# Kernel optimization log

Measured on AMD Instinct MI355X. Metric: run time of the kernel, lower is better.

Reference implementation:

```python
import jax, jax.numpy as jnp
import numpy as np

H = 16  # hidden_size
D = 32  # input_size == output_size
B = 2048
T = 512


def _leaky(x):
    return jnp.where(x >= 0, x, 0.01 * x)  # nn.LeakyReLU default slope


def _lstm_cell(x, h, c, Wih, Whh, bih, bhh):
    # torch.nn.LSTMCell gate order: i, f, g, o
    g = x @ Wih.T + h @ Whh.T + bih + bhh  # [B, 4H]
    i, f, gg, o = jnp.split(g, 4, axis=-1)
    i = jax.nn.sigmoid(i)
    f = jax.nn.sigmoid(f)
    gg = jnp.tanh(gg)
    o = jax.nn.sigmoid(o)
    c = f * c + i * gg
    h = o * jnp.tanh(c)
    return h, c


def setup_inputs() -> dict:
    key = jax.random.key(0)
    ks = jax.random.split(key, 20)
    s = 1.0 / np.sqrt(H)
    u = lambda k, shape: jax.random.uniform(k, shape, jnp.float32, -s, s)
    return {
        "seq": jax.random.normal(ks[0], (B, T, D), jnp.float32),
        "pre_w1": u(ks[1], (H, D)), "pre_b1": u(ks[2], (H,)),
        "pre_w2": u(ks[3], (H, H)), "pre_b2": u(ks[4], (H,)),
        "pre_w3": u(ks[5], (H, H)), "pre_b3": u(ks[6], (H,)),
        "enc_Wih": u(ks[7], (4 * H, H)), "enc_Whh": u(ks[8], (4 * H, H)),
        "enc_bih": u(ks[9], (4 * H,)), "enc_bhh": u(ks[10], (4 * H,)),
        "h2l_w1": u(ks[11], (H, H)), "h2l_b1": u(ks[12], (H,)),
        "h2l_w2": u(ks[13], (H, H)), "h2l_b2": u(ks[14], (H,)),
        "post_w": u(ks[15], (D, H)), "post_b": u(ks[16], (D,)),
    }


def reference(seq, pre_w1, pre_b1, pre_w2, pre_b2, pre_w3, pre_b3,
              enc_Wih, enc_Whh, enc_bih, enc_bhh,
              h2l_w1, h2l_b1, h2l_w2, h2l_b2, post_w, post_b):
    Bx = seq.shape[0]
    # pre MLP: Linear -> LeakyReLU -> Linear -> LeakyReLU -> Linear
    x = _leaky(seq @ pre_w1.T + pre_b1)
    x = _leaky(x @ pre_w2.T + pre_b2)
    x = x @ pre_w3.T + pre_b3  # [B, T, H]

    start0 = x[:, -1, :]
    h0 = jnp.zeros((Bx, H), seq.dtype)
    c0 = jnp.zeros((Bx, H), seq.dtype)

    # encoder loop over time (serial)
    def enc_step(carry, xt):
        h, c = carry
        h, c = _lstm_cell(xt, h, c, enc_Wih, enc_Whh, enc_bih, enc_bhh)
        return (h, c), None

    (h, c), _ = jax.lax.scan(enc_step, (h0, c0), jnp.swapaxes(x, 0, 1))

    # decoder loop (note: source reuses self.encoder cell here)
    def dec_step(carry, _):
        h, c, start = carry
        h, c = _lstm_cell(start, h, c, enc_Wih, enc_Whh, enc_bih, enc_bhh)
        start = _leaky(h @ h2l_w1.T + h2l_b1) @ h2l_w2.T + h2l_b2
        out = h @ post_w.T + post_b  # [B, D]
        return (h, c, start), out

    _, outs = jax.lax.scan(dec_step, (h, c, start0), None, length=seq.shape[1])
    # outputs[:, -1 - i] = out_i  ->  reverse time, then [B, T, D]
    outputs = jnp.swapaxes(outs[::-1], 0, 1)
    return (outputs, outputs)
```

## Files before the change

kernel.cpp:

```cpp
#include <hip/hip_runtime.h>

#define T_LEN 512
#define OSTRIDE ((size_t)2048 * 512 * 32)

typedef float v2f __attribute__((ext_vector_type(2)));
#define PKFMA(a, b, c) __builtin_elementwise_fma((a), (b), (c))

__device__ __forceinline__ float rlf(float v, int l) {
  return __int_as_float(__builtin_amdgcn_readlane(__float_as_int(v), l));
}
#define QB(v, pat) __int_as_float(__builtin_amdgcn_mov_dpp(__float_as_int(v), (pat), 0xF, 0xF, false))

__global__ __launch_bounds__(64) void setup_kernel(
    const float* __restrict__ Wih, const float* __restrict__ bih,
    const float* __restrict__ bhh, const float* __restrict__ w3,
    const float* __restrict__ b3, float* __restrict__ Wz,
    float* __restrict__ Bz) {
  const int g = threadIdx.x;
  const float sK = ((g >> 4) == 2) ? 2.0f : -1.0f;
  float acc[16];
#pragma unroll
  for (int k = 0; k < 16; ++k) acc[k] = 0.f;
  float bz = bih[g] + bhh[g];
#pragma unroll
  for (int j = 0; j < 16; ++j) {
    const float wij = Wih[g * 16 + j];
#pragma unroll
    for (int k = 0; k < 16; ++k)
      acc[k] = __builtin_fmaf(wij, w3[j * 16 + k], acc[k]);
    bz = __builtin_fmaf(wij, b3[j], bz);
  }
#pragma unroll
  for (int k = 0; k < 16; ++k) Wz[g * 16 + k] = sK * acc[k];
  Bz[g] = sK * bz;
}

__global__ __launch_bounds__(256) void prenet_y2_kernel(
    const float* __restrict__ seq,
    const float* __restrict__ w1, const float* __restrict__ b1,
    const float* __restrict__ w2, const float* __restrict__ b2,
    const float* __restrict__ w3, const float* __restrict__ b3,
    float* __restrict__ y2g, float* __restrict__ xstart) {
  const int tid = threadIdx.x;
  const size_t r = (size_t)blockIdx.x * 256 + tid;

  const float* sp = seq + r * 32;
  float in[32];
#pragma unroll
  for (int q = 0; q < 8; ++q) {
    float4 v = ((const float4*)sp)[q];
    in[q * 4 + 0] = v.x;
    in[q * 4 + 1] = v.y;
    in[q * 4 + 2] = v.z;
    in[q * 4 + 3] = v.w;
  }

  float y1[16];
#pragma unroll
  for (int j = 0; j < 16; ++j) {
    float a0 = b1[j], a1 = 0.f, a2 = 0.f, a3 = 0.f;
#pragma unroll
    for (int k = 0; k < 32; k += 4) {
      a0 = __builtin_fmaf(w1[j * 32 + k + 0], in[k + 0], a0);
      a1 = __builtin_fmaf(w1[j * 32 + k + 1], in[k + 1], a1);
      a2 = __builtin_fmaf(w1[j * 32 + k + 2], in[k + 2], a2);
      a3 = __builtin_fmaf(w1[j * 32 + k + 3], in[k + 3], a3);
    }
    float s = (a0 + a1) + (a2 + a3);
    y1[j] = s >= 0.f ? s : 0.01f * s;
  }

  float y2[16];
#pragma unroll
  for (int j = 0; j < 16; ++j) {
    float a0 = b2[j], a1 = 0.f, a2 = 0.f, a3 = 0.f;
#pragma unroll
    for (int k = 0; k < 16; k += 4) {
      a0 = __builtin_fmaf(w2[j * 16 + k + 0], y1[k + 0], a0);
      a1 = __builtin_fmaf(w2[j * 16 + k + 1], y1[k + 1], a1);
      a2 = __builtin_fmaf(w2[j * 16 + k + 2], y1[k + 2], a2);
      a3 = __builtin_fmaf(w2[j * 16 + k + 3], y1[k + 3], a3);
    }
    float s = (a0 + a1) + (a2 + a3);
    y2[j] = s >= 0.f ? s : 0.01f * s;
  }

  float* op = y2g + r * 16;
#pragma unroll
  for (int q = 0; q < 4; ++q)
    ((float4*)op)[q] = make_float4(y2[q * 4 + 0], y2[q * 4 + 1],
                                   y2[q * 4 + 2], y2[q * 4 + 3]);

  if ((r & (T_LEN - 1)) == (T_LEN - 1)) {
    float y3[16];
#pragma unroll
    for (int j = 0; j < 16; ++j) {
      float a0 = b3[j], a1 = 0.f, a2 = 0.f, a3 = 0.f;
#pragma unroll
      for (int k = 0; k < 16; k += 4) {
        a0 = __builtin_fmaf(w3[j * 16 + k + 0], y2[k + 0], a0);
        a1 = __builtin_fmaf(w3[j * 16 + k + 1], y2[k + 1], a1);
        a2 = __builtin_fmaf(w3[j * 16 + k + 2], y2[k + 2], a2);
        a3 = __builtin_fmaf(w3[j * 16 + k + 3], y2[k + 3], a3);
      }
      y3[j] = (a0 + a1) + (a2 + a3);
    }
    float* xs = xstart + (r >> 9) * 16;
#pragma unroll
    for (int q = 0; q < 4; ++q)
      ((float4*)xs)[q] = make_float4(y3[q * 4 + 0], y3[q * 4 + 1],
                                     y3[q * 4 + 2], y3[q * 4 + 3]);
  }
}

#define ACTBODY()                                                           \
  do {                                                                      \
    float ee = __expf(g);                                                   \
    float rr = __builtin_amdgcn_rcpf(1.0f + ee);                            \
    float act = __builtin_fmaf(sa, rr, sb);                                 \
    float ii = QB(act, 0x00);                                               \
    float ff = QB(act, 0x55);                                               \
    float gg = QB(act, 0xAA);                                               \
    float oo = QB(act, 0xFF);                                               \
    c = __builtin_fmaf(ff, c, ii * gg);                                     \
    float th = __builtin_fmaf(                                              \
        -2.0f, __builtin_amdgcn_rcpf(1.0f + __expf(c + c)), 1.0f);          \
    h = oo * th;                                                            \
    _Pragma("unroll") for (int m = 0; m < 8; ++m) {                         \
      hk2[m].x = rlf(h, 8 * m);                                             \
      hk2[m].y = rlf(h, 8 * m + 4);                                         \
    }                                                                       \
  } while (0)

#define CELLZ(ZV)                                                           \
  do {                                                                      \
    v2f A, Bv;                                                              \
    A.x = (ZV); A.y = 0.f; Bv.x = 0.f; Bv.y = 0.f;                          \
    _Pragma("unroll") for (int m = 0; m < 8; m += 2) {                      \
      A = PKFMA(whh2[m], hk2[m], A);                                        \
      Bv = PKFMA(whh2[m + 1], hk2[m + 1], Bv);                              \
    }                                                                       \
    float g = (A.x + A.y) + (Bv.x + Bv.y);                                  \
    ACTBODY();                                                              \
  } while (0)

#define CELL(WX2, XA2, BB)                                                  \
  do {                                                                      \
    v2f A, Bv;                                                              \
    A.x = (BB); A.y = 0.f; Bv.x = 0.f; Bv.y = 0.f;                          \
    _Pragma("unroll") for (int m = 0; m < 8; m += 2) {                      \
      A = PKFMA(WX2[m], XA2[m], A);                                         \
      Bv = PKFMA(WX2[m + 1], XA2[m + 1], Bv);                               \
    }                                                                       \
    _Pragma("unroll") for (int m = 0; m < 8; m += 2) {                      \
      A = PKFMA(whh2[m], hk2[m], A);                                        \
      Bv = PKFMA(whh2[m + 1], hk2[m + 1], Bv);                              \
    }                                                                       \
    float g = (A.x + A.y) + (Bv.x + Bv.y);                                  \
    ACTBODY();                                                              \
  } while (0)

#define ZGEMV(YQ, OUTV)                                                     \
  do {                                                                      \
    v2f A, Bv;                                                              \
    A.x = bz; A.y = 0.f; Bv.x = 0.f; Bv.y = 0.f;                            \
    _Pragma("unroll") for (int q = 0; q < 4; ++q) {                         \
      float4 v = (YQ)[q];                                                   \
      v2f ylo, yhi;                                                         \
      ylo.x = v.x; ylo.y = v.y; yhi.x = v.z; yhi.y = v.w;                   \
      A = PKFMA(wz2[2 * q + 0], ylo, A);                                    \
      Bv = PKFMA(wz2[2 * q + 1], yhi, Bv);                                  \
    }                                                                       \
    OUTV = (A.x + A.y) + (Bv.x + Bv.y);                                     \
  } while (0)

__global__ __launch_bounds__(256, 2) void lstm_rec_z_kernel(
    const float* __restrict__ Whh, const float* __restrict__ Wih,
    const float* __restrict__ bih, const float* __restrict__ bhh,
    const float* __restrict__ hw1, const float* __restrict__ hb1,
    const float* __restrict__ hw2, const float* __restrict__ hb2,
    const float* __restrict__ pw, const float* __restrict__ pb,
    const float* __restrict__ Wz, const float* __restrict__ Bz,
    const float* __restrict__ y2g, const float* __restrict__ xstart,
    float* __restrict__ out) {
  const int lane = threadIdx.x & 63;
  const int bu =
      __builtin_amdgcn_readfirstlane(blockIdx.x * 4 + (threadIdx.x >> 6));
  const int hr = lane >> 2;
  const int gi = (lane & 3) * 16 + hr;
  const bool isT = (lane & 3) == 2;

  const float sK = isT ? 2.0f : -1.0f;
  const float sa = isT ? -2.0f : 1.0f;
  const float sb = isT ? 1.0f : 0.0f;

  v2f whh2[8];
#pragma unroll
  for (int m = 0; m < 8; ++m) {
    whh2[m].x = Whh[gi * 16 + 2 * m + 0] * sK;
    whh2[m].y = Whh[gi * 16 + 2 * m + 1] * sK;
  }

  v2f wz2[8];
  {
    const float4* wzv = (const float4*)(Wz + gi * 16);
#pragma unroll
    for (int q = 0; q < 4; ++q) {
      float4 v = wzv[q];
      wz2[2 * q + 0].x = v.x;
      wz2[2 * q + 0].y = v.y;
      wz2[2 * q + 1].x = v.z;
      wz2[2 * q + 1].y = v.w;
    }
  }
  const float bz = Bz[gi];

  float h = 0.f, c = 0.f;
  v2f hk2[8];
#pragma unroll
  for (int m = 0; m < 8; ++m) { hk2[m].x = 0.f; hk2[m].y = 0.f; }

  const float4* yb = (const float4*)(y2g + (size_t)bu * (T_LEN * 16));
  float4 yq[4][4];
#pragma unroll
  for (int u = 0; u < 4; ++u) {
#pragma unroll
    for (int q = 0; q < 4; ++q) yq[u][q] = yb[u * 4 + q];
  }
  __builtin_amdgcn_sched_barrier(0);

  for (int t0 = 0; t0 < T_LEN; t0 += 4) {
#pragma unroll
    for (int u = 0; u < 4; ++u) {
      float zv;
      ZGEMV(yq[u], zv);
      CELLZ(zv);
      int tn = t0 + u + 4;
      tn = tn < T_LEN ? tn : (T_LEN - 1);
#pragma unroll
      for (int q = 0; q < 4; ++q) yq[u][q] = yb[(size_t)tn * 4 + q];
      __builtin_amdgcn_sched_barrier(0);
    }
  }

  v2f wih2[8];
#pragma unroll
  for (int m = 0; m < 8; ++m) {
    wih2[m].x = Wih[gi * 16 + 2 * m + 0] * sK;
    wih2[m].y = Wih[gi * 16 + 2 * m + 1] * sK;
  }
  const float bias = (bih[gi] + bhh[gi]) * sK;

  const int mrow = (lane < 32) ? lane : (lane & 15);
  const float* msrc = (lane < 32) ? (pw + mrow * 16) : (hw1 + mrow * 16);
  const float mbias = (lane < 32) ? pb[mrow] : hb1[mrow];
  const float sl = (lane < 32) ? 1.0f : 0.01f;
  v2f mr2[8];
#pragma unroll
  for (int m = 0; m < 8; ++m) {
    mr2[m].x = msrc[2 * m + 0];
    mr2[m].y = msrc[2 * m + 1];
  }

  float Mr[16];
#pragma unroll
  for (int k = 0; k < 16; ++k) Mr[k] = 0.f;
#pragma unroll
  for (int j = 0; j < 16; ++j) {
    const float wj = (j & 1) ? wih2[j >> 1].y : wih2[j >> 1].x;
#pragma unroll
    for (int k = 0; k < 16; ++k)
      Mr[k] = __builtin_fmaf(wj, hw2[j * 16 + k], Mr[k]);
  }
  float mbias2 = bias;
#pragma unroll
  for (int j = 0; j < 16; ++j) {
    const float wj = (j & 1) ? wih2[j >> 1].y : wih2[j >> 1].x;
    mbias2 = __builtin_fmaf(wj, hb2[j], mbias2);
  }
  v2f Mr2[8];
#pragma unroll
  for (int m = 0; m < 8; ++m) {
    Mr2[m].x = Mr[2 * m + 0];
    Mr2[m].y = Mr[2 * m + 1];
  }

  v2f xk2[8];
  {
    const float* src = xstart + (size_t)bu * 16;
#pragma unroll
    for (int m = 0; m < 8; ++m) {
      xk2[m].x = src[2 * m + 0];
      xk2[m].y = src[2 * m + 1];
    }
  }

  const size_t obase = (size_t)bu * (T_LEN * 32) + (lane & 31);

  CELL(wih2, xk2, bias);

  for (int t = 0; t < T_LEN; ++t) {
    v2f P, Q;
    P.x = mbias; P.y = 0.f; Q.x = 0.f; Q.y = 0.f;
#pragma unroll
    for (int m = 0; m < 8; m += 2) {
      P = PKFMA(mr2[m], hk2[m], P);
      Q = PKFMA(mr2[m + 1], hk2[m + 1], Q);
    }
    float y0 = (P.x + P.y) + (Q.x + Q.y);
    float yv = fmaxf(y0, y0 * sl);

    if (lane < 32) {
      const size_t off = obase + (size_t)(T_LEN - 1 - t) * 32;
      out[off] = yv;
      out[off + OSTRIDE] = yv;
    }

    if (t + 1 < T_LEN) {
      v2f uk2[8];
#pragma unroll
      for (int m = 0; m < 8; ++m) {
        uk2[m].x = rlf(yv, 32 + 2 * m + 0);
        uk2[m].y = rlf(yv, 32 + 2 * m + 1);
      }
      CELL(Mr2, uk2, mbias2);
    }
  }
}

__device__ __forceinline__ void prenet_row(
    const float* __restrict__ sp,
    const float* __restrict__ w1, const float* __restrict__ b1,
    const float* __restrict__ w2, const float* __restrict__ b2,
    const float* __restrict__ w3, const float* __restrict__ b3,
    float y3[16]) {
  float in[32];
#pragma unroll
  for (int q = 0; q < 8; ++q) {
    float4 v = ((const float4*)sp)[q];
    in[q * 4 + 0] = v.x;
    in[q * 4 + 1] = v.y;
    in[q * 4 + 2] = v.z;
    in[q * 4 + 3] = v.w;
  }
  float y1[16];
#pragma unroll
  for (int j = 0; j < 16; ++j) {
    float a0 = b1[j], a1 = 0.f, a2 = 0.f, a3 = 0.f;
#pragma unroll
    for (int k = 0; k < 32; k += 4) {
      a0 = __builtin_fmaf(w1[j * 32 + k + 0], in[k + 0], a0);
      a1 = __builtin_fmaf(w1[j * 32 + k + 1], in[k + 1], a1);
      a2 = __builtin_fmaf(w1[j * 32 + k + 2], in[k + 2], a2);
      a3 = __builtin_fmaf(w1[j * 32 + k + 3], in[k + 3], a3);
    }
    float s = (a0 + a1) + (a2 + a3);
    y1[j] = s >= 0.f ? s : 0.01f * s;
  }
  float y2[16];
#pragma unroll
  for (int j = 0; j < 16; ++j) {
    float a0 = b2[j], a1 = 0.f, a2 = 0.f, a3 = 0.f;
#pragma unroll
    for (int k = 0; k < 16; k += 4) {
      a0 = __builtin_fmaf(w2[j * 16 + k + 0], y1[k + 0], a0);
      a1 = __builtin_fmaf(w2[j * 16 + k + 1], y1[k + 1], a1);
      a2 = __builtin_fmaf(w2[j * 16 + k + 2], y1[k + 2], a2);
      a3 = __builtin_fmaf(w2[j * 16 + k + 3], y1[k + 3], a3);
    }
    float s = (a0 + a1) + (a2 + a3);
    y2[j] = s >= 0.f ? s : 0.01f * s;
  }
#pragma unroll
  for (int j = 0; j < 16; ++j) {
    float a0 = b3[j], a1 = 0.f, a2 = 0.f, a3 = 0.f;
#pragma unroll
    for (int k = 0; k < 16; k += 4) {
      a0 = __builtin_fmaf(w3[j * 16 + k + 0], y2[k + 0], a0);
      a1 = __builtin_fmaf(w3[j * 16 + k + 1], y2[k + 1], a1);
      a2 = __builtin_fmaf(w3[j * 16 + k + 2], y2[k + 2], a2);
      a3 = __builtin_fmaf(w3[j * 16 + k + 3], y2[k + 3], a3);
    }
    y3[j] = (a0 + a1) + (a2 + a3);
  }
}

__global__ __launch_bounds__(256) void prenet_kernel(
    const float* __restrict__ seq,
    const float* __restrict__ w1, const float* __restrict__ b1,
    const float* __restrict__ w2, const float* __restrict__ b2,
    const float* __restrict__ w3, const float* __restrict__ b3,
    float* __restrict__ xws) {
  const size_t r = (size_t)blockIdx.x * 256 + threadIdx.x;
  float y3[16];
  prenet_row(seq + r * 32, w1, b1, w2, b2, w3, b3, y3);
  float* op = xws + r * 16;
#pragma unroll
  for (int q = 0; q < 4; ++q)
    ((float4*)op)[q] =
        make_float4(y3[q * 4 + 0], y3[q * 4 + 1], y3[q * 4 + 2], y3[q * 4 + 3]);
}

__global__ __launch_bounds__(256, 2) void lstm_rec_kernel(
    const float* __restrict__ Wih, const float* __restrict__ Whh,
    const float* __restrict__ bih, const float* __restrict__ bhh,
    const float* __restrict__ hw1, const float* __restrict__ hb1,
    const float* __restrict__ hw2, const float* __restrict__ hb2,
    const float* __restrict__ pw, const float* __restrict__ pb,
    const float* __restrict__ xws, float* __restrict__ out) {
  const int lane = threadIdx.x & 63;
  const int bu =
      __builtin_amdgcn_readfirstlane(blockIdx.x * 4 + (threadIdx.x >> 6));
  const int hr = lane >> 2;
  const int gi = (lane & 3) * 16 + hr;
  const bool isT = (lane & 3) == 2;

  const float sK = isT ? 2.0f : -1.0f;
  const float sa = isT ? -2.0f : 1.0f;
  const float sb = isT ? 1.0f : 0.0f;

  v2f wih2[8], whh2[8];
#pragma unroll
  for (int m = 0; m < 8; ++m) {
    wih2[m].x = Wih[gi * 16 + 2 * m + 0] * sK;
    wih2[m].y = Wih[gi * 16 + 2 * m + 1] * sK;
    whh2[m].x = Whh[gi * 16 + 2 * m + 0] * sK;
    whh2[m].y = Whh[gi * 16 + 2 * m + 1] * sK;
  }
  const float bias = (bih[gi] + bhh[gi]) * sK;

  float h = 0.f, c = 0.f;
  v2f hk2[8];
#pragma unroll
  for (int m = 0; m < 8; ++m) { hk2[m].x = 0.f; hk2[m].y = 0.f; }

  const float* xb = xws + (size_t)bu * (T_LEN * 16);

  v2f xA2[8], xB2[8];
#pragma unroll
  for (int m = 0; m < 8; ++m) {
    xA2[m].x = xb[2 * m + 0];
    xA2[m].y = xb[2 * m + 1];
  }
  for (int t = 0; t < T_LEN; t += 2) {
    const float* n1 = xb + (size_t)(t + 1) * 16;
#pragma unroll
    for (int m = 0; m < 8; ++m) {
      xB2[m].x = n1[2 * m + 0];
      xB2[m].y = n1[2 * m + 1];
    }
    CELL(wih2, xA2, bias);
    const int t2 = (t + 2 < T_LEN) ? (t + 2) : (T_LEN - 1);
    const float* n2 = xb + (size_t)t2 * 16;
#pragma unroll
    for (int m = 0; m < 8; ++m) {
      xA2[m].x = n2[2 * m + 0];
      xA2[m].y = n2[2 * m + 1];
    }
    CELL(wih2, xB2, bias);
  }

  const int mrow = (lane < 32) ? lane : (lane & 15);
  const float* msrc = (lane < 32) ? (pw + mrow * 16) : (hw1 + mrow * 16);
  const float mbias = (lane < 32) ? pb[mrow] : hb1[mrow];
  const float sl = (lane < 32) ? 1.0f : 0.01f;
  v2f mr2[8];
#pragma unroll
  for (int m = 0; m < 8; ++m) {
    mr2[m].x = msrc[2 * m + 0];
    mr2[m].y = msrc[2 * m + 1];
  }

  float Mr[16];
#pragma unroll
  for (int k = 0; k < 16; ++k) Mr[k] = 0.f;
#pragma unroll
  for (int j = 0; j < 16; ++j) {
    const float wj = (j & 1) ? wih2[j >> 1].y : wih2[j >> 1].x;
#pragma unroll
    for (int k = 0; k < 16; ++k)
      Mr[k] = __builtin_fmaf(wj, hw2[j * 16 + k], Mr[k]);
  }
  float mbias2 = bias;
#pragma unroll
  for (int j = 0; j < 16; ++j) {
    const float wj = (j & 1) ? wih2[j >> 1].y : wih2[j >> 1].x;
    mbias2 = __builtin_fmaf(wj, hb2[j], mbias2);
  }
  v2f Mr2[8];
#pragma unroll
  for (int m = 0; m < 8; ++m) {
    Mr2[m].x = Mr[2 * m + 0];
    Mr2[m].y = Mr[2 * m + 1];
  }

  v2f xk2[8];
  {
    const float* src = xb + (size_t)(T_LEN - 1) * 16;
#pragma unroll
    for (int m = 0; m < 8; ++m) {
      xk2[m].x = src[2 * m + 0];
      xk2[m].y = src[2 * m + 1];
    }
  }

  const size_t obase = (size_t)bu * (T_LEN * 32) + (lane & 31);

  CELL(wih2, xk2, bias);

  for (int t = 0; t < T_LEN; ++t) {
    v2f P, Q;
    P.x = mbias; P.y = 0.f; Q.x = 0.f; Q.y = 0.f;
#pragma unroll
    for (int m = 0; m < 8; m += 2) {
      P = PKFMA(mr2[m], hk2[m], P);
      Q = PKFMA(mr2[m + 1], hk2[m + 1], Q);
    }
    float y0 = (P.x + P.y) + (Q.x + Q.y);
    float yv = fmaxf(y0, y0 * sl);

    if (lane < 32) {
      const size_t off = obase + (size_t)(T_LEN - 1 - t) * 32;
      out[off] = yv;
      out[off + OSTRIDE] = yv;
    }

    if (t + 1 < T_LEN) {
      v2f uk2[8];
#pragma unroll
      for (int m = 0; m < 8; ++m) {
        uk2[m].x = rlf(yv, 32 + 2 * m + 0);
        uk2[m].y = rlf(yv, 32 + 2 * m + 1);
      }
      CELL(Mr2, uk2, mbias2);
    }
  }
}

extern "C" void kernel_launch(void* const* d_in, const int* in_sizes, int n_in,
                              void* d_out, int out_size, void* d_ws, size_t ws_size,
                              hipStream_t stream) {
  const float* seq = (const float*)d_in[0];
  const float* pre_w1 = (const float*)d_in[1];
  const float* pre_b1 = (const float*)d_in[2];
  const float* pre_w2 = (const float*)d_in[3];
  const float* pre_b2 = (const float*)d_in[4];
  const float* pre_w3 = (const float*)d_in[5];
  const float* pre_b3 = (const float*)d_in[6];
  const float* enc_Wih = (const float*)d_in[7];
  const float* enc_Whh = (const float*)d_in[8];
  const float* enc_bih = (const float*)d_in[9];
  const float* enc_bhh = (const float*)d_in[10];
  const float* h2l_w1 = (const float*)d_in[11];
  const float* h2l_b1 = (const float*)d_in[12];
  const float* h2l_w2 = (const float*)d_in[13];
  const float* h2l_b2 = (const float*)d_in[14];
  const float* post_w = (const float*)d_in[15];
  const float* post_b = (const float*)d_in[16];

  const size_t y2bytes = (size_t)2048 * 512 * 16 * 4;
  const size_t xsbytes = (size_t)2048 * 16 * 4;
  const size_t wzbytes = 64 * 16 * 4;
  const size_t need = y2bytes + xsbytes + wzbytes + 64 * 4;

  if (ws_size >= need) {
    float* y2g = (float*)d_ws;
    float* xstart = (float*)((char*)d_ws + y2bytes);
    float* Wz = (float*)((char*)d_ws + y2bytes + xsbytes);
    float* Bz = (float*)((char*)d_ws + y2bytes + xsbytes + wzbytes);

    setup_kernel<<<dim3(1), dim3(64), 0, stream>>>(
        enc_Wih, enc_bih, enc_bhh, pre_w3, pre_b3, Wz, Bz);

    prenet_y2_kernel<<<dim3(4096), dim3(256), 0, stream>>>(
        seq, pre_w1, pre_b1, pre_w2, pre_b2, pre_w3, pre_b3, y2g, xstart);

    lstm_rec_z_kernel<<<dim3(512), dim3(256), 0, stream>>>(
        enc_Whh, enc_Wih, enc_bih, enc_bhh, h2l_w1, h2l_b1, h2l_w2, h2l_b2,
        post_w, post_b, Wz, Bz, y2g, xstart, (float*)d_out);
  } else {
    float* xws = (float*)d_ws;

    prenet_kernel<<<dim3(4096), dim3(256), 0, stream>>>(
        seq, pre_w1, pre_b1, pre_w2, pre_b2, pre_w3, pre_b3, xws);

    lstm_rec_kernel<<<dim3(512), dim3(256), 0, stream>>>(
        enc_Wih, enc_Whh, enc_bih, enc_bhh, h2l_w1, h2l_b1, h2l_w2, h2l_b2,
        post_w, post_b, xws, (float*)d_out);
  }
}
```

Before: 720.7 us.

## Interleave two independent batch rows per wavefront in LSTM recurrence kernel

Each wavefront now runs two batch rows' LSTM recurrences side by side, with separate h/c state and register rings, so the two dependent chains can fill each other's latency gaps (ILP) rather than relying on occupancy. The z GEMV for the next timestep is computed one step ahead, so it overlaps with the current cell update. The grid is halved to 256 blocks with launch bounds of 1 block per SM, which raises register use per thread and lowers occupancy in exchange for more independent work per wave.

```diff
diff --git a/kernel.cpp b/kernel.cpp
--- a/kernel.cpp
+++ b/kernel.cpp
@@ -113,68 +113,74 @@
   }
 }
 
-#define ACTBODY()                                                           \
+#define ACT_P(G, H, C, HK)                                                  \
   do {                                                                      \
-    float ee = __expf(g);                                                   \
-    float rr = __builtin_amdgcn_rcpf(1.0f + ee);                            \
-    float act = __builtin_fmaf(sa, rr, sb);                                 \
-    float ii = QB(act, 0x00);                                               \
-    float ff = QB(act, 0x55);                                               \
-    float gg = QB(act, 0xAA);                                               \
-    float oo = QB(act, 0xFF);                                               \
-    c = __builtin_fmaf(ff, c, ii * gg);                                     \
-    float th = __builtin_fmaf(                                              \
-        -2.0f, __builtin_amdgcn_rcpf(1.0f + __expf(c + c)), 1.0f);          \
-    h = oo * th;                                                            \
+    float ee_ = __expf(G);                                                  \
+    float rr_ = __builtin_amdgcn_rcpf(1.0f + ee_);                          \
+    float act_ = __builtin_fmaf(sa, rr_, sb);                               \
+    float ii_ = QB(act_, 0x00);                                             \
+    float ff_ = QB(act_, 0x55);                                             \
+    float gg_ = QB(act_, 0xAA);                                             \
+    float oo_ = QB(act_, 0xFF);                                             \
+    C = __builtin_fmaf(ff_, C, ii_ * gg_);                                  \
+    float th_ = __builtin_fmaf(                                             \
+        -2.0f, __builtin_amdgcn_rcpf(1.0f + __expf(C + C)), 1.0f);          \
+    H = oo_ * th_;                                                          \
     _Pragma("unroll") for (int m = 0; m < 8; ++m) {                         \
-      hk2[m].x = rlf(h, 8 * m);                                             \
-      hk2[m].y = rlf(h, 8 * m + 4);                                         \
+      HK[m].x = rlf(H, 8 * m);                                              \
+      HK[m].y = rlf(H, 8 * m + 4);                                          \
     }                                                                       \
   } while (0)
 
-#define CELLZ(ZV)                                                           \
+#define CELLZ_P(ZV, H, C, HK)                                               \
   do {                                                                      \
-    v2f A, Bv;                                                              \
-    A.x = (ZV); A.y = 0.f; Bv.x = 0.f; Bv.y = 0.f;                          \
+    v2f A_, B_;                                                             \
+    A_.x = (ZV); A_.y = 0.f; B_.x = 0.f; B_.y = 0.f;                        \
     _Pragma("unroll") for (int m = 0; m < 8; m += 2) {                      \
-      A = PKFMA(whh2[m], hk2[m], A);                                        \
-      Bv = PKFMA(whh2[m + 1], hk2[m + 1], Bv);                              \
+      A_ = PKFMA(whh2[m], HK[m], A_);                                       \
+      B_ = PKFMA(whh2[m + 1], HK[m + 1], B_);                               \
     }                                                                       \
-    float g = (A.x + A.y) + (Bv.x + Bv.y);                                  \
-    ACTBODY();                                                              \
+    float g_ = (A_.x + A_.y) + (B_.x + B_.y);                               \
+    ACT_P(g_, H, C, HK);                                                    \
   } while (0)
 
-#define CELL(WX2, XA2, BB)                                                  \
+#define CELL_P(WX2, XA2, BB, H, C, HK)                                      \
   do {                                                                      \
-    v2f A, Bv;                                                              \
-    A.x = (BB); A.y = 0.f; Bv.x = 0.f; Bv.y = 0.f;                          \
+    v2f A_, B_;                                                             \
+    A_.x = (BB); A_.y = 0.f; B_.x = 0.f; B_.y = 0.f;                        \
     _Pragma("unroll") for (int m = 0; m < 8; m += 2) {                      \
-      A = PKFMA(WX2[m], XA2[m], A);                                         \
-      Bv = PKFMA(WX2[m + 1], XA2[m + 1], Bv);                               \
+      A_ = PKFMA(WX2[m], XA2[m], A_);                                       \
+      B_ = PKFMA(WX2[m + 1], XA2[m + 1], B_);                               \
     }                                                                       \
     _Pragma("unroll") for (int m = 0; m < 8; m += 2) {                      \
-      A = PKFMA(whh2[m], hk2[m], A);                                        \
-      Bv = PKFMA(whh2[m + 1], hk2[m + 1], Bv);                              \
+      A_ = PKFMA(whh2[m], HK[m], A_);                                       \
+      B_ = PKFMA(whh2[m + 1], HK[m + 1], B_);                               \
     }                                                                       \
-    float g = (A.x + A.y) + (Bv.x + Bv.y);                                  \
-    ACTBODY();                                                              \
+    float g_ = (A_.x + A_.y) + (B_.x + B_.y);                               \
+    ACT_P(g_, H, C, HK);                                                    \
   } while (0)
 
-#define ZGEMV(YQ, OUTV)                                                     \
+#define ZGEMV_P(YQ, OUTV)                                                   \
   do {                                                                      \
-    v2f A, Bv;                                                              \
-    A.x = bz; A.y = 0.f; Bv.x = 0.f; Bv.y = 0.f;                            \
+    v2f A_, B_;                                                             \
+    A_.x = bz; A_.y = 0.f; B_.x = 0.f; B_.y = 0.f;                          \
     _Pragma("unroll") for (int q = 0; q < 4; ++q) {                         \
-      float4 v = (YQ)[q];                                                   \
-      v2f ylo, yhi;                                                         \
-      ylo.x = v.x; ylo.y = v.y; yhi.x = v.z; yhi.y = v.w;                   \
-      A = PKFMA(wz2[2 * q + 0], ylo, A);                                    \
-      Bv = PKFMA(wz2[2 * q + 1], yhi, Bv);                                  \
+      float4 v_ = (YQ)[q];                                                  \
+      v2f ylo_, yhi_;                                                       \
+      ylo_.x = v_.x; ylo_.y = v_.y; yhi_.x = v_.z; yhi_.y = v_.w;           \
+      A_ = PKFMA(wz2[2 * q + 0], ylo_, A_);                                 \
+      B_ = PKFMA(wz2[2 * q + 1], yhi_, B_);                                 \
     }                                                                       \
-    OUTV = (A.x + A.y) + (Bv.x + Bv.y);                                     \
+    OUTV = (A_.x + A_.y) + (B_.x + B_.y);                                   \
   } while (0)
 
-__global__ __launch_bounds__(256, 2) void lstm_rec_z_kernel(
+#define LDY(RING, YB, ROW)                                                  \
+  do {                                                                      \
+    _Pragma("unroll") for (int q = 0; q < 4; ++q)                           \
+      RING[q] = (YB)[(size_t)(ROW) * 4 + q];                                \
+  } while (0)
+
+__global__ __launch_bounds__(256, 1) void lstm_rec_z2_kernel(
     const float* __restrict__ Whh, const float* __restrict__ Wih,
     const float* __restrict__ bih, const float* __restrict__ bhh,
     const float* __restrict__ hw1, const float* __restrict__ hb1,
@@ -184,8 +190,10 @@
     const float* __restrict__ y2g, const float* __restrict__ xstart,
     float* __restrict__ out) {
   const int lane = threadIdx.x & 63;
-  const int bu =
-      __builtin_amdgcn_readfirstlane(blockIdx.x * 4 + (threadIdx.x >> 6));
+  const int wid = threadIdx.x >> 6;
+  const int bu0 =
+      __builtin_amdgcn_readfirstlane(blockIdx.x * 8 + wid * 2);
+  const int bu1 = bu0 + 1;
   const int hr = lane >> 2;
   const int gi = (lane & 3) * 16 + hr;
   const bool isT = (lane & 3) == 2;
@@ -215,31 +223,43 @@
   }
   const float bz = Bz[gi];
 
-  float h = 0.f, c = 0.f;
-  v2f hk2[8];
-#pragma unroll
-  for (int m = 0; m < 8; ++m) { hk2[m].x = 0.f; hk2[m].y = 0.f; }
-
-  const float4* yb = (const float4*)(y2g + (size_t)bu * (T_LEN * 16));
-  float4 yq[4][4];
+  float hA = 0.f, cA = 0.f, hB = 0.f, cB = 0.f;
+  v2f hkA[8], hkB[8];
+#pragma unroll
+  for (int m = 0; m < 8; ++m) {
+    hkA[m].x = 0.f; hkA[m].y = 0.f;
+    hkB[m].x = 0.f; hkB[m].y = 0.f;
+  }
+
+  const float4* ybA = (const float4*)(y2g + (size_t)bu0 * (T_LEN * 16));
+  const float4* ybB = (const float4*)(y2g + (size_t)bu1 * (T_LEN * 16));
+  float4 yqA[4][4], yqB[4][4];
 #pragma unroll
   for (int u = 0; u < 4; ++u) {
-#pragma unroll
-    for (int q = 0; q < 4; ++q) yq[u][q] = yb[u * 4 + q];
+    LDY(yqA[u], ybA, u);
+    LDY(yqB[u], ybB, u);
   }
   __builtin_amdgcn_sched_barrier(0);
 
+  float zcA, zcB;
+  ZGEMV_P(yqA[0], zcA);
+  ZGEMV_P(yqB[0], zcB);
+
   for (int t0 = 0; t0 < T_LEN; t0 += 4) {
 #pragma unroll
     for (int u = 0; u < 4; ++u) {
-      float zv;
-      ZGEMV(yq[u], zv);
-      CELLZ(zv);
+      float znA, znB;
+      ZGEMV_P(yqA[(u + 1) & 3], znA);
+      ZGEMV_P(yqB[(u + 1) & 3], znB);
+      CELLZ_P(zcA, hA, cA, hkA);
+      CELLZ_P(zcB, hB, cB, hkB);
       int tn = t0 + u + 4;
       tn = tn < T_LEN ? tn : (T_LEN - 1);
-#pragma unroll
-      for (int q = 0; q < 4; ++q) yq[u][q] = yb[(size_t)tn * 4 + q];
+      LDY(yqA[u], ybA, tn);
+      LDY(yqB[u], ybB, tn);
       __builtin_amdgcn_sched_barrier(0);
+      zcA = znA;
+      zcB = znB;
     }
   }
 
@@ -285,45 +305,61 @@
     Mr2[m].y = Mr[2 * m + 1];
   }
 
-  v2f xk2[8];
+  v2f xkA[8], xkB[8];
   {
-    const float* src = xstart + (size_t)bu * 16;
+    const float* sA = xstart + (size_t)bu0 * 16;
+    const float* sB = xstart + (size_t)bu1 * 16;
 #pragma unroll
     for (int m = 0; m < 8; ++m) {
-      xk2[m].x = src[2 * m + 0];
-      xk2[m].y = src[2 * m + 1];
-    }
-  }
-
-  const size_t obase = (size_t)bu * (T_LEN * 32) + (lane & 31);
-
-  CELL(wih2, xk2, bias);
+      xkA[m].x = sA[2 * m + 0];
+      xkA[m].y = sA[2 * m + 1];
+      xkB[m].x = sB[2 * m + 0];
+      xkB[m].y = sB[2 * m + 1];
+    }
+  }
+
+  const size_t obaseA = (size_t)bu0 * (T_LEN * 32) + (lane & 31);
+  const size_t obaseB = (size_t)bu1 * (T_LEN * 32) + (lane & 31);
+
+  CELL_P(wih2, xkA, bias, hA, cA, hkA);
+  CELL_P(wih2, xkB, bias, hB, cB, hkB);
 
   for (int t = 0; t < T_LEN; ++t) {
-    v2f P, Q;
-    P.x = mbias; P.y = 0.f; Q.x = 0.f; Q.y = 0.f;
+    v2f PA, QA, PB, QBv;
+    PA.x = mbias; PA.y = 0.f; QA.x = 0.f; QA.y = 0.f;
+    PB.x = mbias; PB.y = 0.f; QBv.x = 0.f; QBv.y = 0.f;
 #pragma unroll
     for (int m = 0; m < 8; m += 2) {
-      P = PKFMA(mr2[m], hk2[m], P);
-      Q = PKFMA(mr2[m + 1], hk2[m + 1], Q);
-    }
-    float y0 = (P.x + P.y) + (Q.x + Q.y);
-    float yv = fmaxf(y0, y0 * sl);
+      PA = PKFMA(mr2[m], hkA[m], PA);
+      QA = PKFMA(mr2[m + 1], hkA[m + 1], QA);
+      PB = PKFMA(mr2[m], hkB[m], PB);
+      QBv = PKFMA(mr2[m + 1], hkB[m + 1], QBv);
+    }
+    float y0A = (PA.x + PA.y) + (QA.x + QA.y);
+    float y0B = (PB.x + PB.y) + (QBv.x + QBv.y);
+    float yvA = fmaxf(y0A, y0A * sl);
+    float yvB = fmaxf(y0B, y0B * sl);
 
     if (lane < 32) {
-      const size_t off = obase + (size_t)(T_LEN - 1 - t) * 32;
-      out[off] = yv;
-      out[off + OSTRIDE] = yv;
+      const size_t offA = obaseA + (size_t)(T_LEN - 1 - t) * 32;
+      const size_t offB = obaseB + (size_t)(T_LEN - 1 - t) * 32;
+      out[offA] = yvA;
+      out[offA + OSTRIDE] = yvA;
+      out[offB] = yvB;
+      out[offB + OSTRIDE] = yvB;
     }
 
     if (t + 1 < T_LEN) {
-      v2f uk2[8];
+      v2f ukA[8], ukB[8];
 #pragma unroll
       for (int m = 0; m < 8; ++m) {
-        uk2[m].x = rlf(yv, 32 + 2 * m + 0);
-        uk2[m].y = rlf(yv, 32 + 2 * m + 1);
+        ukA[m].x = rlf(yvA, 32 + 2 * m + 0);
+        ukA[m].y = rlf(yvA, 32 + 2 * m + 1);
+        ukB[m].x = rlf(yvB, 32 + 2 * m + 0);
+        ukB[m].y = rlf(yvB, 32 + 2 * m + 1);
       }
-      CELL(Mr2, uk2, mbias2);
+      CELL_P(Mr2, ukA, mbias2, hA, cA, hkA);
+      CELL_P(Mr2, ukB, mbias2, hB, cB, hkB);
     }
   }
 }
@@ -449,7 +485,7 @@
       xB2[m].x = n1[2 * m + 0];
       xB2[m].y = n1[2 * m + 1];
     }
-    CELL(wih2, xA2, bias);
+    CELL_P(wih2, xA2, bias, h, c, hk2);
     const int t2 = (t + 2 < T_LEN) ? (t + 2) : (T_LEN - 1);
     const float* n2 = xb + (size_t)t2 * 16;
 #pragma unroll
@@ -457,7 +493,7 @@
       xA2[m].x = n2[2 * m + 0];
       xA2[m].y = n2[2 * m + 1];
     }
-    CELL(wih2, xB2, bias);
+    CELL_P(wih2, xB2, bias, h, c, hk2);
   }
 
   const int mrow = (lane < 32) ? lane : (lane & 15);
@@ -506,7 +542,7 @@
 
   const size_t obase = (size_t)bu * (T_LEN * 32) + (lane & 31);
 
-  CELL(wih2, xk2, bias);
+  CELL_P(wih2, xk2, bias, h, c, hk2);
 
   for (int t = 0; t < T_LEN; ++t) {
     v2f P, Q;
@@ -532,7 +568,7 @@
         uk2[m].x = rlf(yv, 32 + 2 * m + 0);
         uk2[m].y = rlf(yv, 32 + 2 * m + 1);
       }
-      CELL(Mr2, uk2, mbias2);
+      CELL_P(Mr2, uk2, mbias2, h, c, hk2);
     }
   }
 }
@@ -575,7 +611,7 @@
     prenet_y2_kernel<<<dim3(4096), dim3(256), 0, stream>>>(
         seq, pre_w1, pre_b1, pre_w2, pre_b2, pre_w3, pre_b3, y2g, xstart);
 
-    lstm_rec_z_kernel<<<dim3(512), dim3(256), 0, stream>>>(
+    lstm_rec_z2_kernel<<<dim3(256), dim3(256), 0, stream>>>(
         enc_Whh, enc_Wih, enc_bih, enc_bhh, h2l_w1, h2l_b1, h2l_w2, h2l_b2,
         post_w, post_b, Wz, Bz, y2g, xstart, (float*)d_out);
   } else {
```

Measured after the change: 854.8 us. 18.6% more time.
